# Optimization experiments

Hardware: AMD Instinct MI355X
Metric: run time of the kernel (lower is better)

Reference implementation:

```python
import jax, jax.numpy as jnp
import numpy as np

N_U, N_I, D, L, Q, N_E, B = 100000, 50000, 128, 2, 5, 1000000, 4096
TEMP, LAMBDA1, DROPOUT = 0.2, 0.2, 0.2


def setup_inputs() -> dict:
    key = jax.random.key(0)
    ks = jax.random.split(key, 14)
    s = 1.0 / np.sqrt(D)
    E_u_0 = jax.random.normal(ks[0], (N_U, D), dtype=jnp.float32) * s
    E_i_0 = jax.random.normal(ks[1], (N_I, D), dtype=jnp.float32) * s
    W_s = jax.random.normal(ks[2], (L, D, D), dtype=jnp.float32) * s
    # truncated-SVD factors of adj_norm (rank Q)
    u_mul_s = jax.random.normal(ks[3], (N_U, Q), dtype=jnp.float32) * 0.01
    v_mul_s = jax.random.normal(ks[4], (N_I, Q), dtype=jnp.float32) * 0.01
    ut = jax.random.normal(ks[5], (Q, N_U), dtype=jnp.float32) * 0.01
    vt = jax.random.normal(ks[6], (Q, N_I), dtype=jnp.float32) * 0.01
    # normalized bipartite adjacency in COO form
    adj_rows = jax.random.randint(ks[7], (N_E,), 0, N_U)
    adj_cols = jax.random.randint(ks[8], (N_E,), 0, N_I)
    adj_vals = jax.random.uniform(ks[9], (N_E,), dtype=jnp.float32) * 0.01
    uids = jax.random.randint(ks[10], (B,), 0, N_U)
    iids = jax.random.randint(ks[11], (B,), 0, N_I)
    pos = jax.random.randint(ks[12], (B,), 0, N_I)
    neg = jax.random.randint(ks[13], (B,), 0, N_I)
    return dict(E_u_0=E_u_0, E_i_0=E_i_0, W_s=W_s, u_mul_s=u_mul_s,
                v_mul_s=v_mul_s, ut=ut, vt=vt, adj_vals=adj_vals,
                adj_rows=adj_rows, adj_cols=adj_cols,
                uids=uids, iids=iids, pos=pos, neg=neg)


def _normalize(x):
    n = jnp.linalg.norm(x, axis=1, keepdims=True)
    return x / jnp.maximum(n, 1e-12)


def reference(E_u_0, E_i_0, W_s, u_mul_s, v_mul_s, ut, vt, adj_vals,
              adj_rows, adj_cols, uids, iids, pos, neg):
    act = lambda x: jax.nn.leaky_relu(x, 0.5)
    rkey = jax.random.key(42)
    keep_p = 1.0 - DROPOUT
    E_u, E_i = E_u_0, E_i_0
    E_u_sum, E_i_sum = E_u_0, E_i_0
    Z_u_list, Z_i_list, G_u_list, G_i_list = [], [], [], []
    for layer in range(L):
        k1, k2, rkey = jax.random.split(rkey, 3)
        # two independent sparse dropouts (as in the original, one per spmm)
        v1 = jnp.where(jax.random.bernoulli(k1, keep_p, (N_E,)), adj_vals / keep_p, 0.0)
        v2 = jnp.where(jax.random.bernoulli(k2, keep_p, (N_E,)), adj_vals / keep_p, 0.0)
        # spmm: gather item/user rows, scale by edge val, scatter-add
        Z_u = act(jax.ops.segment_sum(v1[:, None] * E_i[adj_cols], adj_rows, num_segments=N_U))
        Z_i = act(jax.ops.segment_sum(v2[:, None] * E_u[adj_rows], adj_cols, num_segments=N_I))
        # SVD global propagation (low-rank)
        G_u = act(u_mul_s @ (vt @ E_i))
        G_i = act(v_mul_s @ (ut @ E_u))
        E_u = Z_u + E_u
        E_i = Z_i + E_i
        E_u_sum = E_u_sum + E_u
        E_i_sum = E_i_sum + E_i
        Z_u_list.append(Z_u); Z_i_list.append(Z_i)
        G_u_list.append(G_u); G_i_list.append(G_i)

    # InfoNCE contrastive loss per layer
    loss_s = jnp.float32(0.0)
    for l in range(L):
        km1, km2, rkey = jax.random.split(rkey, 3)
        u_mask = (jax.random.uniform(km1, (uids.shape[0],)) > 0.5).astype(jnp.float32)
        gnn_u = _normalize(Z_u_list[l][uids])
        hyper_u = _normalize(G_u_list[l][uids]) @ W_s[l]
        pos_u = jnp.exp(jnp.sum(gnn_u * hyper_u, axis=1) / TEMP)
        neg_u = jnp.sum(jnp.exp(gnn_u @ hyper_u.T / TEMP), axis=1)
        loss_s = loss_s + jnp.sum(-jnp.log(pos_u / (neg_u + 1e-8) + 1e-8) * u_mask)
        i_mask = (jax.random.uniform(km2, (iids.shape[0],)) > 0.5).astype(jnp.float32)
        gnn_i = _normalize(Z_i_list[l][iids])
        hyper_i = _normalize(G_i_list[l][iids]) @ W_s[l]
        pos_i = jnp.exp(jnp.sum(gnn_i * hyper_i, axis=1) / TEMP)
        neg_i = jnp.sum(jnp.exp(gnn_i @ hyper_i.T / TEMP), axis=1)
        loss_s = loss_s + jnp.sum(-jnp.log(pos_i / (neg_i + 1e-8) + 1e-8) * i_mask)

    # BPR loss (vectorized over the per-user loop, one pos/neg per user)
    u_emb = E_u_sum[uids]
    ps = jnp.sum(u_emb * E_i_sum[pos], axis=1)
    ns = jnp.sum(u_emb * E_i_sum[neg], axis=1)
    loss_r = jnp.sum(jax.nn.relu(1.0 - ps + ns)) / B

    loss = loss_r + LAMBDA1 * loss_s
    return loss, loss_r, loss_s
```

## Files before the change

kernel.cpp:

```cpp
#include <hip/hip_runtime.h>
#include <cstdint>
#include <cstddef>

static const int CNU = 100000;
static const int CNI = 50000;
static const int CD  = 128;
static const int CL  = 2;
static const int CQ  = 5;
static const int CNE = 1000000;
static const int CB  = 4096;
#define INV_TEMP 5.0f
#define LAMBDA1 0.2f
#define KEEP_P 0.8f
#define CAP_R 40
#define CAP_C 56
#define NBU 391
#define NBI 196
#define NXCD 8
#define SEGCAP_U 512
#define SEGCAP_I 896
#define QSCALE 655280.0f
#define QSTEP  1.5258902e-6f

typedef unsigned short ushortT;
typedef __attribute__((ext_vector_type(8))) short bf16x8;
typedef __attribute__((ext_vector_type(4))) float f32x4;

__host__ __device__ inline uint32_t rotl32(uint32_t v, int r){ return (v<<r)|(v>>(32-r)); }

__host__ __device__ inline void threefry2x32(uint32_t k0, uint32_t k1, uint32_t x0, uint32_t x1,
                                             uint32_t* o0, uint32_t* o1){
  uint32_t ks0=k0, ks1=k1, ks2=k0^k1^0x1BD11BDAu;
  x0+=ks0; x1+=ks1;
#define TF_R(r) { x0+=x1; x1=rotl32(x1,(r)); x1^=x0; }
  TF_R(13) TF_R(15) TF_R(26) TF_R(6)   x0+=ks1; x1+=ks2+1u;
  TF_R(17) TF_R(29) TF_R(16) TF_R(24)  x0+=ks2; x1+=ks0+2u;
  TF_R(13) TF_R(15) TF_R(26) TF_R(6)   x0+=ks0; x1+=ks1+3u;
  TF_R(17) TF_R(29) TF_R(16) TF_R(24)  x0+=ks1; x1+=ks2+4u;
  TF_R(13) TF_R(15) TF_R(26) TF_R(6)   x0+=ks2; x1+=ks0+5u;
#undef TF_R
  *o0=x0; *o1=x1;
}

static void split3(uint32_t k0, uint32_t k1, uint32_t o[6]){
  uint32_t a,b;
  threefry2x32(k0,k1,0u,3u,&a,&b); o[0]=a; o[3]=b;
  threefry2x32(k0,k1,1u,4u,&a,&b); o[1]=a; o[4]=b;
  threefry2x32(k0,k1,2u,5u,&a,&b); o[2]=a; o[5]=b;
}

__device__ inline float u01(uint32_t b){
  return __uint_as_float((b>>9)|0x3f800000u) - 1.0f;
}
__device__ inline float lrelu(float x){ return x>0.0f ? x : 0.5f*x; }
__device__ inline uint32_t f2bf(float f){
  uint32_t u = __float_as_uint(f);
  u += 0x7fffu + ((u>>16)&1u);
  return u>>16;
}
__device__ inline float bf2f(ushortT s){
  return __uint_as_float(((uint32_t)s)<<16);
}
__device__ inline float bflo(int x){ return __uint_as_float(((uint32_t)x)<<16); }
__device__ inline float bfhi(int x){ return __uint_as_float(((uint32_t)x)&0xffff0000u); }

__device__ inline int keep_draw(uint32_t k0, uint32_t k1, uint32_t e){
  const uint32_t H = CNE/2;
  uint32_t c0 = (e<H)? e : e-H;
  uint32_t r0,r1;
  threefry2x32(k0,k1,c0,c0+H,&r0,&r1);
  uint32_t rw = (e<H)? r0 : r1;
  return (rw < 3435974144u) ? 1 : 0;
}

__device__ inline uint32_t xcc_id(){
  return __builtin_amdgcn_s_getreg((3<<11) | (0<<6) | 20) & (NXCD-1);
}


__global__ void k_cvt(const float* __restrict__ Eu, const float* __restrict__ Ei,
                      ushortT* __restrict__ Eub, ushortT* __restrict__ Eib){
  size_t i = (size_t)blockIdx.x*blockDim.x + threadIdx.x;
  const size_t nu = (size_t)CNU*CD/8;
  const size_t ni = (size_t)CNI*CD/8;
  const float* src; ushortT* dst; size_t j;
  if(i < nu){ src=Eu; dst=Eub; j=i; }
  else if(i < nu+ni){ src=Ei; dst=Eib; j=i-nu; }
  else return;
  const float4* s = (const float4*)(src + j*8);
  float4 a = s[0], b = s[1];
  int4 o;
  o.x = (int)(f2bf(a.x) | (f2bf(a.y)<<16));
  o.y = (int)(f2bf(a.z) | (f2bf(a.w)<<16));
  o.z = (int)(f2bf(b.x) | (f2bf(b.y)<<16));
  o.w = (int)(f2bf(b.z) | (f2bf(b.w)<<16));
  ((int4*)dst)[j] = o;
}

__global__ void k_binfill(const int* __restrict__ rows, const int* __restrict__ cols,
                          const float* __restrict__ vals,
                          int* __restrict__ bcnt_u, int* __restrict__ bcnt_i,
                          int2* __restrict__ bin_u, int2* __restrict__ bin_i,
                          uint32_t ka00, uint32_t ka01, uint32_t ka10, uint32_t ka11,
                          uint32_t kb00, uint32_t kb01, uint32_t kb10, uint32_t kb11){
  int e = blockIdx.x*blockDim.x + threadIdx.x;
  if(e >= CNE) return;
  int xid = (int)xcc_id();
  int r = rows[e], c = cols[e];
  float v = vals[e] * (1.0f/KEEP_P);
  uint32_t q = (uint32_t)(v*QSCALE + 0.5f);
  if(q > 8191u) q = 8191u;
  uint32_t ue = (uint32_t)e;
  uint32_t d0r = keep_draw(ka00, ka01, ue);
  uint32_t d1r = keep_draw(ka10, ka11, ue);
  uint32_t d0c = keep_draw(kb00, kb01, ue);
  uint32_t d1c = keep_draw(kb10, kb11, ue);
  {
    int seg = (r>>8)*NXCD + xid;
    int slot = atomicAdd(&bcnt_u[seg*16], 1);
    if(slot < SEGCAP_U){
      int2 p; p.x = c | ((r&255)<<17); p.y = (int)((d0r<<14)|(d1r<<13)|q);
      bin_u[(size_t)seg*SEGCAP_U + slot] = p;
    }
  }
  {
    int seg = (c>>8)*NXCD + xid;
    int slot = atomicAdd(&bcnt_i[seg*16], 1);
    if(slot < SEGCAP_I){
      int2 p; p.x = r | ((c&255)<<17); p.y = (int)((d0c<<14)|(d1c<<13)|q);
      bin_i[(size_t)seg*SEGCAP_I + slot] = p;
    }
  }
}

__global__ __launch_bounds__(256) void k_build(
    const int* __restrict__ bcnt_u, const int2* __restrict__ bin_u,
    const int* __restrict__ bcnt_i, const int2* __restrict__ bin_i,
    int* __restrict__ cnt_u, uint32_t* __restrict__ pad_u,
    int* __restrict__ cnt_i, uint32_t* __restrict__ pad_i){
  __shared__ int rc[256];
  __shared__ uint32_t lpad[256*CAP_C];
  bool user = blockIdx.x < NBU;
  int bin  = user ? blockIdx.x : blockIdx.x - NBU;
  int N    = user ? CNU : CNI;
  int CAP  = user ? CAP_R : CAP_C;
  int scap = user ? SEGCAP_U : SEGCAP_I;
  const int*  bcnt = user ? bcnt_u : bcnt_i;
  const int2* bino = user ? bin_u : bin_i;
  int* cnto = user ? cnt_u : cnt_i;
  uint32_t* pado = user ? pad_u : pad_i;
  int base = bin<<8;
  int nrows = N - base; if(nrows > 256) nrows = 256;
  int t = threadIdx.x;
  rc[t] = 0;
  __syncthreads();
#pragma unroll
  for(int sgi=0; sgi<NXCD; sgi++){
    int seg = bin*NXCD + sgi;
    int cnt = bcnt[seg*16];
    if(cnt > scap) cnt = scap;
    const int2* bins = bino + (size_t)seg*scap;
    for(int i=t; i<cnt; i+=256){
      int2 p = bins[i];
      int local = ((uint32_t)p.x) >> 17;
      uint32_t gi = (uint32_t)p.x & 0x1FFFFu;
      int slot = atomicAdd(&rc[local], 1);
      if(slot < CAP) lpad[local*CAP + slot] = (gi<<15) | (uint32_t)p.y;
    }
  }
  __syncthreads();
  if(t < nrows){ int n = rc[t]; cnto[base+t] = n>CAP ? CAP : n; }
  int tot4 = (nrows*CAP) >> 2;
  int4* dst = (int4*)(pado + (size_t)base*CAP);
  const int4* src = (const int4*)lpad;
  for(int i4=t; i4<tot4; i4+=256) dst[i4] = src[i4];
}


__global__ __launch_bounds__(256) void k_spmm(
    const int* __restrict__ cnt_u, const uint32_t* __restrict__ pad_u,
    const int* __restrict__ cnt_i, const uint32_t* __restrict__ pad_i,
    const ushortT* __restrict__ Eu_in, const ushortT* __restrict__ Ei_in,
    ushortT* __restrict__ Eu_out, ushortT* __restrict__ Ei_out, int layer){
  __shared__ int2 meta[4][64];
  int wid = threadIdx.x>>6;
  int w = blockIdx.x*4 + wid;
  if(w >= CNU+CNI) return;
  int lane = threadIdx.x & 63;
  bool user = (w < CNU);
  const int*      cnt = user ? cnt_u : cnt_i;
  const uint32_t* pad = user ? pad_u : pad_i;
  int cap             = user ? CAP_R : CAP_C;
  const ushortT* X    = user ? Ei_in : Eu_in;
  const ushortT* Ein  = user ? Eu_in : Ei_in;
  ushortT* Eout       = user ? Eu_out : Ei_out;
  int row = user ? w : (w - CNU);
  int n = cnt[row]; if(n > cap) n = cap;
  const uint32_t* base = pad + (size_t)row*cap;
  int s = lane>>4, l16 = lane&15;

  int2 mm = make_int2(0,0);
  if(lane < n){
    uint32_t mw = base[lane];
    uint32_t keep = (mw >> (14-layer)) & 1u;
    float vv = keep ? (float)(mw & 0x1FFFu) * QSTEP : 0.0f;
    mm.x = (int)(mw >> 15);
    mm.y = __float_as_int(vv);
  }
  meta[wid][lane] = mm;

  float acc[8];
#pragma unroll
  for(int k=0;k<8;k++) acc[k]=0.0f;
  int np = (n+3)>>2;
  for(int i=0;i<np;i++){
    int2 md = meta[wid][i*4+s];
    float vv = __int_as_float(md.y);
    if(vv != 0.0f){
      int4 xv = *(const int4*)(X + (size_t)md.x*CD + l16*8);
      acc[0] += vv*bflo(xv.x); acc[1] += vv*bfhi(xv.x);
      acc[2] += vv*bflo(xv.y); acc[3] += vv*bfhi(xv.y);
      acc[4] += vv*bflo(xv.z); acc[5] += vv*bfhi(xv.z);
      acc[6] += vv*bflo(xv.w); acc[7] += vv*bfhi(xv.w);
    }
  }
#pragma unroll
  for(int k=0;k<8;k++){
    acc[k] += __shfl_xor(acc[k], 16);
    acc[k] += __shfl_xor(acc[k], 32);
  }
  if(s==0){
    int4 ev = *(const int4*)(Ein + (size_t)row*CD + l16*8);
    int4 o;
    o.x = (int)(f2bf(bflo(ev.x)+lrelu(acc[0])) | (f2bf(bfhi(ev.x)+lrelu(acc[1]))<<16));
    o.y = (int)(f2bf(bflo(ev.y)+lrelu(acc[2])) | (f2bf(bfhi(ev.y)+lrelu(acc[3]))<<16));
    o.z = (int)(f2bf(bflo(ev.z)+lrelu(acc[4])) | (f2bf(bfhi(ev.z)+lrelu(acc[5]))<<16));
    o.w = (int)(f2bf(bflo(ev.w)+lrelu(acc[6])) | (f2bf(bfhi(ev.w)+lrelu(acc[7]))<<16));
    *(int4*)(Eout + (size_t)row*CD + l16*8) = o;
  }
}

#define NCH_I 196
#define NCH_U 391
__global__ __launch_bounds__(256) void k_vtE2(const float* __restrict__ vt, const float* __restrict__ ut,
                       const ushortT* __restrict__ Ei, const ushortT* __restrict__ Eu,
                       float* __restrict__ Tu, float* __restrict__ Ti){
  bool sideU = blockIdx.x >= NCH_I;
  int chunk = sideU ? (blockIdx.x - NCH_I) : blockIdx.x;
  const float* M   = sideU ? ut : vt;
  const ushortT* X = sideU ? Eu : Ei;
  float* T         = sideU ? Ti : Tu;
  int N            = sideU ? CNU : CNI;
  int base = chunk*256;
  int t = threadIdx.x;
  int rg = t>>4, dg = t&15;
  float acc[CQ][8];
#pragma unroll
  for(int q=0;q<CQ;q++)
#pragma unroll
    for(int j=0;j<8;j++) acc[q][j]=0.0f;
  for(int rr=rg; rr<256; rr+=16){
    int r = base+rr;
    if(r >= N) break;
    int4 xv = ((const int4*)(X + (size_t)r*CD))[dg];
    float x[8];
    x[0]=bflo(xv.x); x[1]=bfhi(xv.x); x[2]=bflo(xv.y); x[3]=bfhi(xv.y);
    x[4]=bflo(xv.z); x[5]=bfhi(xv.z); x[6]=bflo(xv.w); x[7]=bfhi(xv.w);
#pragma unroll
    for(int q=0;q<CQ;q++){
      float m = M[(size_t)q*N + r];
#pragma unroll
      for(int j=0;j<8;j++) acc[q][j] += m*x[j];
    }
  }
#pragma unroll
  for(int q=0;q<CQ;q++)
#pragma unroll
    for(int j=0;j<8;j++){
      float v = acc[q][j];
      v += __shfl_xor(v, 16);
      v += __shfl_xor(v, 32);
      acc[q][j] = v;
    }
  __shared__ float red[4][656];
  int wv = t>>6;
  int lane = t&63;
  if(lane < 16){
#pragma unroll
    for(int q=0;q<CQ;q++)
#pragma unroll
      for(int j=0;j<8;j++)
        red[wv][dg*41 + q*8 + j] = acc[q][j];
  }
  __syncthreads();
  for(int i=t; i<CQ*128; i+=256){
    int q = i>>7, rem = i&127;
    int dgi = rem>>3, j = rem&7;
    int idx = dgi*41 + q*8 + j;
    float s = red[0][idx] + red[1][idx] + red[2][idx] + red[3][idx];
    atomicAdd(&T[i], s);
  }
}

__global__ void k_hyper2(const int* __restrict__ uids, const int* __restrict__ iids,
                         const float* __restrict__ u_mul_s, const float* __restrict__ v_mul_s,
                         const float* __restrict__ Tu, const float* __restrict__ Ti,
                         const float* __restrict__ W,
                         ushortT* __restrict__ hu, ushortT* __restrict__ hi){
  int side = blockIdx.x >> 12;
  int b    = blockIdx.x & 4095;
  const int* ids = side ? iids : uids;
  const float* ms = side ? v_mul_s : u_mul_s;
  const float* T  = side ? Ti : Tu;
  ushortT* outp = side ? hi : hu;
  int d = threadIdx.x;
  int id = ids[b];
  float g = 0.0f;
#pragma unroll
  for(int q=0;q<CQ;q++) g += ms[(size_t)id*CQ+q]*T[q*128+d];
  g = lrelu(g);
  __shared__ float red[128];
  __shared__ float gn[128];
  red[d]=g*g; __syncthreads();
  for(int s=64;s>0;s>>=1){ if(d<s) red[d]+=red[d+s]; __syncthreads(); }
  float nrm = sqrtf(red[0]);
  gn[d] = g / fmaxf(nrm, 1e-12f);
  __syncthreads();
  float h=0.0f;
  for(int k=0;k<128;k++) h += gn[k]*W[k*128+d];
  outp[(size_t)b*128+d]=(ushortT)f2bf(h);
}

__global__ void k_gnn2(const int* __restrict__ uids, const int* __restrict__ iids,
                       const ushortT* __restrict__ EuN, const ushortT* __restrict__ EuO,
                       const ushortT* __restrict__ EiN, const ushortT* __restrict__ EiO,
                       ushortT* __restrict__ gu, ushortT* __restrict__ gi){
  int side = blockIdx.x >> 12;
  int b    = blockIdx.x & 4095;
  const int* ids = side ? iids : uids;
  const ushortT* En = side ? EiN : EuN;
  const ushortT* Eo = side ? EiO : EuO;
  ushortT* outp = side ? gi : gu;
  int d = threadIdx.x;
  int id = ids[b];
  float z = bf2f(En[(size_t)id*CD+d]) - bf2f(Eo[(size_t)id*CD+d]);
  __shared__ float red[128];
  red[d]=z*z; __syncthreads();
  for(int s=64;s>0;s>>=1){ if(d<s) red[d]+=red[d+s]; __syncthreads(); }
  outp[(size_t)b*CD+d] = (ushortT)f2bf(z / fmaxf(sqrtf(red[0]), 1e-12f));
}

__global__ void k_gacc3(const int* __restrict__ uids, const int* __restrict__ pids,
                        const int* __restrict__ nids,
                        const ushortT* __restrict__ Eu, const ushortT* __restrict__ Ei,
                        float* __restrict__ usum, float* __restrict__ iposb,
                        float* __restrict__ inegb, int init){
  int side = blockIdx.x >> 12;
  int b    = blockIdx.x & 4095;
  const int* ids = (side==0)? uids : (side==1)? pids : nids;
  const ushortT* E = (side==0)? Eu : Ei;
  float* S = (side==0)? usum : (side==1)? iposb : inegb;
  int d = threadIdx.x;
  float v = bf2f(E[(size_t)ids[b]*CD+d]);
  if(init) S[(size_t)b*CD+d]=v;
  else     S[(size_t)b*CD+d]+=v;
}

__global__ __launch_bounds__(256) void k_nce_mfma(const ushortT* __restrict__ gnnb,
                                                  const ushortT* __restrict__ hypb,
                                                  float* __restrict__ neg){
  int c = blockIdx.z;
  const ushortT* G = gnnb + (size_t)c*CB*CD;
  const ushortT* H = hypb + (size_t)c*CB*CD;
  int wid  = threadIdx.x >> 6;
  int lane = threadIdx.x & 63;
  int lr = lane & 15;
  int lk = lane >> 4;
  int rb = blockIdx.x*256 + wid*64;
  int cc = blockIdx.y*512;

  bf16x8 a[4][4];
#pragma unroll
  for(int rt=0;rt<4;rt++)
#pragma unroll
    for(int ks=0;ks<4;ks++)
      a[rt][ks] = *(const bf16x8*)(G + (size_t)(rb+rt*16+lr)*CD + ks*32 + lk*8);

  float rsum[4][4];
#pragma unroll
  for(int rt=0;rt<4;rt++)
#pragma unroll
    for(int r=0;r<4;r++) rsum[rt][r]=0.0f;

  for(int cb=cc; cb<cc+512; cb+=16){
    bf16x8 b[4];
#pragma unroll
    for(int ks=0;ks<4;ks++)
      b[ks] = *(const bf16x8*)(H + (size_t)(cb+lr)*CD + ks*32 + lk*8);
#pragma unroll
    for(int rt=0;rt<4;rt++){
      f32x4 acc = {0.f,0.f,0.f,0.f};
#pragma unroll
      for(int ks=0;ks<4;ks++)
        acc = __builtin_amdgcn_mfma_f32_16x16x32_bf16(a[rt][ks], b[ks], acc, 0,0,0);
#pragma unroll
      for(int r=0;r<4;r++)
        rsum[rt][r] += __expf(acc[r]*INV_TEMP);
    }
  }
#pragma unroll
  for(int rt=0;rt<4;rt++)
#pragma unroll
    for(int r=0;r<4;r++){
      float s = rsum[rt][r];
      s += __shfl_xor(s, 1);
      s += __shfl_xor(s, 2);
      s += __shfl_xor(s, 4);
      s += __shfl_xor(s, 8);
      if(lr==0) atomicAdd(&neg[(size_t)c*CB + rb + rt*16 + lk*4 + r], s);
    }
}

__global__ void k_loss(const ushortT* __restrict__ gnnb, const ushortT* __restrict__ hypb,
                       const float* __restrict__ neg, float* __restrict__ vbuf,
                       uint32_t k0a,uint32_t k0b,uint32_t k1a,uint32_t k1b,
                       uint32_t k2a,uint32_t k2b,uint32_t k3a,uint32_t k3b){
  int idx = blockIdx.x*4 + (threadIdx.x>>6);
  int lane = threadIdx.x & 63;
  const ushortT* g = gnnb + (size_t)idx*CD + lane*2;
  const ushortT* h = hypb + (size_t)idx*CD + lane*2;
  float s = bf2f(g[0])*bf2f(h[0]) + bf2f(g[1])*bf2f(h[1]);
#pragma unroll
  for(int m=32; m; m>>=1) s += __shfl_xor(s, m);
  if(lane==0){
    int c = idx>>12, j = idx&4095;
    uint32_t ka = (c==0)?k0a:(c==1)?k1a:(c==2)?k2a:k3a;
    uint32_t kb = (c==0)?k0b:(c==1)?k1b:(c==2)?k2b:k3b;
    uint32_t jj = (j<2048)? (uint32_t)j : (uint32_t)(j-2048);
    uint32_t r0,r1;
    threefry2x32(ka,kb,jj,jj+2048u,&r0,&r1);
    uint32_t rw = (j<2048)? r0 : r1;
    float mask = (u01(rw) > 0.5f) ? 1.0f : 0.0f;
    float p = __expf(s*INV_TEMP);
    vbuf[idx] = -logf(p/(neg[idx]+1e-8f)+1e-8f) * mask;
  }
}

__global__ void k_bpr(const float* __restrict__ usum, const float* __restrict__ ipos,
                      const float* __restrict__ ineg, float* __restrict__ rbuf){
  int t = threadIdx.x;
  int lane = t & 63, sub = t >> 6;
  int b = blockIdx.x*4 + sub;
  float2 u  = ((const float2*)(usum + (size_t)b*CD))[lane];
  float2 p  = ((const float2*)(ipos + (size_t)b*CD))[lane];
  float2 nn = ((const float2*)(ineg + (size_t)b*CD))[lane];
  float ps = u.x*p.x + u.y*p.y;
  float ns = u.x*nn.x + u.y*nn.y;
  for(int off=32; off; off>>=1){ ps += __shfl_down(ps,off); ns += __shfl_down(ns,off); }
  if(lane==0){
    float v = 1.0f - ps + ns;
    rbuf[b] = v>0.0f ? v : 0.0f;
  }
}

__global__ void k_final(const float* __restrict__ vbuf, const float* __restrict__ rbuf,
                        float* __restrict__ out){
  int t = threadIdx.x;
  float s=0.0f, r=0.0f;
  for(int i=t; i<4*CB; i+=256) s += vbuf[i];
  for(int i=t; i<CB;   i+=256) r += rbuf[i];
  __shared__ float rs[256], rr[256];
  rs[t]=s; rr[t]=r; __syncthreads();
  for(int o=128;o>0;o>>=1){ if(t<o){ rs[t]+=rs[t+o]; rr[t]+=rr[t+o]; } __syncthreads(); }
  if(t==0){
    float loss_s = rs[0];
    float loss_r = rr[0]/(float)CB;
    out[0] = loss_r + LAMBDA1*loss_s;
    out[1] = loss_r;
    out[2] = loss_s;
  }
}

extern "C" void kernel_launch(void* const* d_in, const int* in_sizes, int n_in,
                              void* d_out, int out_size, void* d_ws, size_t ws_size,
                              hipStream_t stream){
  const float* E_u_0   = (const float*)d_in[0];
  const float* E_i_0   = (const float*)d_in[1];
  const float* W_s     = (const float*)d_in[2];
  const float* u_mul_s = (const float*)d_in[3];
  const float* v_mul_s = (const float*)d_in[4];
  const float* ut      = (const float*)d_in[5];
  const float* vt      = (const float*)d_in[6];
  const float* adj_vals= (const float*)d_in[7];
  const int*   adj_rows= (const int*)d_in[8];
  const int*   adj_cols= (const int*)d_in[9];
  const int*   uids    = (const int*)d_in[10];
  const int*   iids    = (const int*)d_in[11];
  const int*   pos_ids = (const int*)d_in[12];
  const int*   neg_ids = (const int*)d_in[13];
  float* out = (float*)d_out;

  float* ws = (float*)d_ws;
  size_t off = 0;
  auto alloc = [&](size_t n){ float* p = ws + off; off += (n+3)&~(size_t)3; return p; };
  ushortT* Eu0b = (ushortT*)alloc((size_t)CNU*CD/2);
  ushortT* Ei0b = (ushortT*)alloc((size_t)CNI*CD/2);
  ushortT* EuA  = (ushortT*)alloc((size_t)CNU*CD/2);
  ushortT* EuB  = (ushortT*)alloc((size_t)CNU*CD/2);
  ushortT* EiA  = (ushortT*)alloc((size_t)CNI*CD/2);
  ushortT* EiB  = (ushortT*)alloc((size_t)CNI*CD/2);
  float* Tu   = alloc(CQ*128);
  float* Ti   = alloc(CQ*128);
  ushortT* gnnb = (ushortT*)alloc(4*(size_t)CB*CD/2);
  ushortT* hypb = (ushortT*)alloc(4*(size_t)CB*CD/2);
  float* usum = alloc((size_t)CB*CD);
  float* iposb= alloc((size_t)CB*CD);
  float* inegb= alloc((size_t)CB*CD);
  float* negb = alloc(4*CB);
  float* vbuf = alloc(4*CB);
  float* rbuf = alloc(CB);
  int* bcnt_u = (int*)alloc((size_t)NBU*NXCD*16);
  int* bcnt_i = (int*)alloc((size_t)NBI*NXCD*16);
  int2* bin_u = (int2*)alloc((size_t)NBU*NXCD*SEGCAP_U*2);
  int2* bin_i = (int2*)alloc((size_t)NBI*NXCD*SEGCAP_I*2);
  int* cnt_u = (int*)alloc(CNU);
  int* cnt_i = (int*)alloc(CNI);
  uint32_t* pad_u = (uint32_t*)alloc((size_t)CNU*CAP_R);
  uint32_t* pad_i = (uint32_t*)alloc((size_t)CNI*CAP_C);

  uint32_t rk0 = 0u, rk1 = 42u;
  uint32_t kd[CL][2][2];
  uint32_t km[4][2];
  for(int l=0;l<CL;l++){
    uint32_t o[6]; split3(rk0,rk1,o);
    kd[l][0][0]=o[0]; kd[l][0][1]=o[1];
    kd[l][1][0]=o[2]; kd[l][1][1]=o[3];
    rk0=o[4]; rk1=o[5];
  }
  for(int l=0;l<CL;l++){
    uint32_t o[6]; split3(rk0,rk1,o);
    km[l*2+0][0]=o[0]; km[l*2+0][1]=o[1];
    km[l*2+1][0]=o[2]; km[l*2+1][1]=o[3];
    rk0=o[4]; rk1=o[5];
  }

  hipMemsetAsync(bcnt_u, 0, (size_t)NBU*NXCD*16*sizeof(int), stream);
  hipMemsetAsync(bcnt_i, 0, (size_t)NBI*NXCD*16*sizeof(int), stream);
  hipMemsetAsync(Tu, 0, CQ*128*sizeof(float), stream);
  hipMemsetAsync(Ti, 0, CQ*128*sizeof(float), stream);
  hipMemsetAsync(negb, 0, 4*CB*sizeof(float), stream);

  {
    size_t tot = ((size_t)CNU+CNI)*CD/8;
    k_cvt<<<(int)((tot+255)/256),256,0,stream>>>(E_u_0, E_i_0, Eu0b, Ei0b);
  }
  k_binfill<<<(CNE+255)/256,256,0,stream>>>(adj_rows, adj_cols, adj_vals,
      bcnt_u, bcnt_i, bin_u, bin_i,
      kd[0][0][0],kd[0][0][1], kd[1][0][0],kd[1][0][1],
      kd[0][1][0],kd[0][1][1], kd[1][1][0],kd[1][1][1]);
  k_build<<<NBU+NBI,256,0,stream>>>(bcnt_u, bin_u, bcnt_i, bin_i,
      cnt_u, pad_u, cnt_i, pad_i);

  k_gacc3<<<3*CB,128,0,stream>>>(uids, pos_ids, neg_ids, Eu0b, Ei0b,
                                 usum, iposb, inegb, 1);

  const ushortT* Eu_cur = Eu0b;
  const ushortT* Ei_cur = Ei0b;
  ushortT* Eu_next_bufs[2] = {EuA, EuB};
  ushortT* Ei_next_bufs[2] = {EiA, EiB};

  for(int l=0;l<CL;l++){
    ushortT* Eu_next = Eu_next_bufs[l];
    ushortT* Ei_next = Ei_next_bufs[l];

    k_spmm<<<(CNU+CNI+3)/4,256,0,stream>>>(
        cnt_u, pad_u, cnt_i, pad_i,
        Eu_cur, Ei_cur, Eu_next, Ei_next, l);

    k_vtE2<<<NCH_I+NCH_U,256,0,stream>>>(vt, ut, Ei_cur, Eu_cur, Tu, Ti);

    const float* Wl = W_s + (size_t)l*CD*CD;
    k_hyper2<<<2*CB,128,0,stream>>>(uids, iids, u_mul_s, v_mul_s, Tu, Ti, Wl,
        hypb + (size_t)(l*2+0)*CB*CD, hypb + (size_t)(l*2+1)*CB*CD);

    k_gnn2<<<2*CB,128,0,stream>>>(uids, iids, Eu_next, Eu_cur, Ei_next, Ei_cur,
        gnnb + (size_t)(l*2+0)*CB*CD, gnnb + (size_t)(l*2+1)*CB*CD);

    Eu_cur = Eu_next; Ei_cur = Ei_next;

    k_gacc3<<<3*CB,128,0,stream>>>(uids, pos_ids, neg_ids, Eu_cur, Ei_cur,
                                   usum, iposb, inegb, 0);

    if(l+1<CL){
      hipMemsetAsync(Tu, 0, CQ*128*sizeof(float), stream);
      hipMemsetAsync(Ti, 0, CQ*128*sizeof(float), stream);
    }
  }

  dim3 gnce(CB/256, CB/512, 4);
  k_nce_mfma<<<gnce,256,0,stream>>>(gnnb, hypb, negb);

  k_loss<<<4*CB/4,256,0,stream>>>(gnnb, hypb, negb, vbuf,
      km[0][0],km[0][1], km[1][0],km[1][1], km[2][0],km[2][1], km[3][0],km[3][1]);
  k_bpr<<<CB/4,256,0,stream>>>(usum, iposb, inegb, rbuf);
  k_final<<<1,256,0,stream>>>(vbuf, rbuf, out);
}
```

Measured before the change: 483.5 us.

## Merge setup, per-layer, and tail stages into fewer heterogeneous-grid kernels

Several small kernels are combined into block-range-dispatched kernels. Bin filling, bf16 conversion and the initial BPR gather become one setup kernel. SpMM and the low-rank vt·E projection share one per-layer kernel, and hyper, gnn-normalisation and the BPR accumulation share another. The loss and BPR kernels are merged, and the separate memsets are folded into two, with the T buffers made per-layer so no re-zeroing is needed between layers. The goal is to cut launch count and inter-kernel idle time and to let independent stages overlap inside one grid. The cost is larger, more divergent kernels and merged memsets that depend on adjacent allocations.

```diff
diff --git a/kernel.cpp b/kernel.cpp
--- a/kernel.cpp
+++ b/kernel.cpp
@@ -21,6 +21,13 @@
 #define SEGCAP_I 896
 #define QSCALE 655280.0f
 #define QSTEP  1.5258902e-6f
+#define NCH_I 196
+#define NCH_U 391
+#define NCH   (NCH_I+NCH_U)
+#define NBF   3907
+#define NCVT  2344
+#define NGA   6144
+#define NSPMM 37500
 
 typedef unsigned short ushortT;
 typedef __attribute__((ext_vector_type(8))) short bf16x8;
@@ -77,59 +84,73 @@
   return __builtin_amdgcn_s_getreg((3<<11) | (0<<6) | 20) & (NXCD-1);
 }
 
-
-__global__ void k_cvt(const float* __restrict__ Eu, const float* __restrict__ Ei,
-                      ushortT* __restrict__ Eub, ushortT* __restrict__ Eib){
-  size_t i = (size_t)blockIdx.x*blockDim.x + threadIdx.x;
-  const size_t nu = (size_t)CNU*CD/8;
-  const size_t ni = (size_t)CNI*CD/8;
-  const float* src; ushortT* dst; size_t j;
-  if(i < nu){ src=Eu; dst=Eub; j=i; }
-  else if(i < nu+ni){ src=Ei; dst=Eib; j=i-nu; }
-  else return;
-  const float4* s = (const float4*)(src + j*8);
-  float4 a = s[0], b = s[1];
-  int4 o;
-  o.x = (int)(f2bf(a.x) | (f2bf(a.y)<<16));
-  o.y = (int)(f2bf(a.z) | (f2bf(a.w)<<16));
-  o.z = (int)(f2bf(b.x) | (f2bf(b.y)<<16));
-  o.w = (int)(f2bf(b.z) | (f2bf(b.w)<<16));
-  ((int4*)dst)[j] = o;
-}
-
-__global__ void k_binfill(const int* __restrict__ rows, const int* __restrict__ cols,
-                          const float* __restrict__ vals,
-                          int* __restrict__ bcnt_u, int* __restrict__ bcnt_i,
-                          int2* __restrict__ bin_u, int2* __restrict__ bin_i,
-                          uint32_t ka00, uint32_t ka01, uint32_t ka10, uint32_t ka11,
-                          uint32_t kb00, uint32_t kb01, uint32_t kb10, uint32_t kb11){
-  int e = blockIdx.x*blockDim.x + threadIdx.x;
-  if(e >= CNE) return;
-  int xid = (int)xcc_id();
-  int r = rows[e], c = cols[e];
-  float v = vals[e] * (1.0f/KEEP_P);
-  uint32_t q = (uint32_t)(v*QSCALE + 0.5f);
-  if(q > 8191u) q = 8191u;
-  uint32_t ue = (uint32_t)e;
-  uint32_t d0r = keep_draw(ka00, ka01, ue);
-  uint32_t d1r = keep_draw(ka10, ka11, ue);
-  uint32_t d0c = keep_draw(kb00, kb01, ue);
-  uint32_t d1c = keep_draw(kb10, kb11, ue);
-  {
-    int seg = (r>>8)*NXCD + xid;
-    int slot = atomicAdd(&bcnt_u[seg*16], 1);
-    if(slot < SEGCAP_U){
-      int2 p; p.x = c | ((r&255)<<17); p.y = (int)((d0r<<14)|(d1r<<13)|q);
-      bin_u[(size_t)seg*SEGCAP_U + slot] = p;
-    }
-  }
-  {
-    int seg = (c>>8)*NXCD + xid;
-    int slot = atomicAdd(&bcnt_i[seg*16], 1);
-    if(slot < SEGCAP_I){
-      int2 p; p.x = r | ((c&255)<<17); p.y = (int)((d0c<<14)|(d1c<<13)|q);
-      bin_i[(size_t)seg*SEGCAP_I + slot] = p;
-    }
+__global__ __launch_bounds__(256) void k_setup(
+    const int* __restrict__ rows, const int* __restrict__ cols,
+    const float* __restrict__ vals,
+    int* __restrict__ bcnt_u, int* __restrict__ bcnt_i,
+    int2* __restrict__ bin_u, int2* __restrict__ bin_i,
+    const float* __restrict__ Euf, const float* __restrict__ Eif,
+    ushortT* __restrict__ Eub, ushortT* __restrict__ Eib,
+    const int* __restrict__ uids, const int* __restrict__ pids, const int* __restrict__ nids,
+    float* __restrict__ usum, float* __restrict__ iposb, float* __restrict__ inegb,
+    uint32_t ka00, uint32_t ka01, uint32_t ka10, uint32_t ka11,
+    uint32_t kb00, uint32_t kb01, uint32_t kb10, uint32_t kb11){
+  int t = threadIdx.x;
+  if(blockIdx.x < NBF){
+    int e = blockIdx.x*256 + t;
+    if(e >= CNE) return;
+    int xid = (int)xcc_id();
+    int r = rows[e], c = cols[e];
+    float v = vals[e] * (1.0f/KEEP_P);
+    uint32_t q = (uint32_t)(v*QSCALE + 0.5f);
+    if(q > 8191u) q = 8191u;
+    uint32_t ue = (uint32_t)e;
+    uint32_t d0r = keep_draw(ka00, ka01, ue);
+    uint32_t d1r = keep_draw(ka10, ka11, ue);
+    uint32_t d0c = keep_draw(kb00, kb01, ue);
+    uint32_t d1c = keep_draw(kb10, kb11, ue);
+    {
+      int seg = (r>>8)*NXCD + xid;
+      int slot = atomicAdd(&bcnt_u[seg*16], 1);
+      if(slot < SEGCAP_U){
+        int2 p; p.x = c | ((r&255)<<17); p.y = (int)((d0r<<14)|(d1r<<13)|q);
+        bin_u[(size_t)seg*SEGCAP_U + slot] = p;
+      }
+    }
+    {
+      int seg = (c>>8)*NXCD + xid;
+      int slot = atomicAdd(&bcnt_i[seg*16], 1);
+      if(slot < SEGCAP_I){
+        int2 p; p.x = r | ((c&255)<<17); p.y = (int)((d0c<<14)|(d1c<<13)|q);
+        bin_i[(size_t)seg*SEGCAP_I + slot] = p;
+      }
+    }
+  } else if(blockIdx.x < NBF+NCVT){
+    const size_t nu = (size_t)CNU*CD/8;
+    const size_t M4 = (size_t)(CNU+CNI)*CD/8;
+    size_t i0 = (size_t)(blockIdx.x - NBF)*256 + t;
+    for(size_t i=i0; i<M4; i += (size_t)NCVT*256){
+      const float* src; ushortT* dst; size_t j;
+      if(i < nu){ src=Euf; dst=Eub; j=i; }
+      else{ src=Eif; dst=Eib; j=i-nu; }
+      const float4* s = (const float4*)(src + j*8);
+      float4 a = s[0], b = s[1];
+      int4 o;
+      o.x = (int)(f2bf(a.x) | (f2bf(a.y)<<16));
+      o.y = (int)(f2bf(a.z) | (f2bf(a.w)<<16));
+      o.z = (int)(f2bf(b.x) | (f2bf(b.y)<<16));
+      o.w = (int)(f2bf(b.z) | (f2bf(b.w)<<16));
+      ((int4*)dst)[j] = o;
+    }
+  } else {
+    int item = (blockIdx.x - NBF - NCVT)*2 + (t>>7);
+    int side = item >> 12;
+    int b    = item & 4095;
+    int d    = t & 127;
+    const int* ids = (side==0)? uids : (side==1)? pids : nids;
+    const float* E = (side==0)? Euf : Eif;
+    float* S = (side==0)? usum : (side==1)? iposb : inegb;
+    S[(size_t)b*CD+d] = E[(size_t)ids[b]*CD+d];
   }
 }
 
@@ -176,194 +197,186 @@
   for(int i4=t; i4<tot4; i4+=256) dst[i4] = src[i4];
 }
 
-
-__global__ __launch_bounds__(256) void k_spmm(
+__global__ __launch_bounds__(256) void k_layer_main(
     const int* __restrict__ cnt_u, const uint32_t* __restrict__ pad_u,
     const int* __restrict__ cnt_i, const uint32_t* __restrict__ pad_i,
     const ushortT* __restrict__ Eu_in, const ushortT* __restrict__ Ei_in,
-    ushortT* __restrict__ Eu_out, ushortT* __restrict__ Ei_out, int layer){
+    ushortT* __restrict__ Eu_out, ushortT* __restrict__ Ei_out,
+    const float* __restrict__ vt, const float* __restrict__ ut,
+    float* __restrict__ Tbuf, int layer){
   __shared__ int2 meta[4][64];
-  int wid = threadIdx.x>>6;
-  int w = blockIdx.x*4 + wid;
-  if(w >= CNU+CNI) return;
-  int lane = threadIdx.x & 63;
-  bool user = (w < CNU);
-  const int*      cnt = user ? cnt_u : cnt_i;
-  const uint32_t* pad = user ? pad_u : pad_i;
-  int cap             = user ? CAP_R : CAP_C;
-  const ushortT* X    = user ? Ei_in : Eu_in;
-  const ushortT* Ein  = user ? Eu_in : Ei_in;
-  ushortT* Eout       = user ? Eu_out : Ei_out;
-  int row = user ? w : (w - CNU);
-  int n = cnt[row]; if(n > cap) n = cap;
-  const uint32_t* base = pad + (size_t)row*cap;
-  int s = lane>>4, l16 = lane&15;
-
-  int2 mm = make_int2(0,0);
-  if(lane < n){
-    uint32_t mw = base[lane];
-    uint32_t keep = (mw >> (14-layer)) & 1u;
-    float vv = keep ? (float)(mw & 0x1FFFu) * QSTEP : 0.0f;
-    mm.x = (int)(mw >> 15);
-    mm.y = __float_as_int(vv);
-  }
-  meta[wid][lane] = mm;
-
-  float acc[8];
-#pragma unroll
-  for(int k=0;k<8;k++) acc[k]=0.0f;
-  int np = (n+3)>>2;
-  for(int i=0;i<np;i++){
-    int2 md = meta[wid][i*4+s];
-    float vv = __int_as_float(md.y);
-    if(vv != 0.0f){
-      int4 xv = *(const int4*)(X + (size_t)md.x*CD + l16*8);
-      acc[0] += vv*bflo(xv.x); acc[1] += vv*bfhi(xv.x);
-      acc[2] += vv*bflo(xv.y); acc[3] += vv*bfhi(xv.y);
-      acc[4] += vv*bflo(xv.z); acc[5] += vv*bfhi(xv.z);
-      acc[6] += vv*bflo(xv.w); acc[7] += vv*bfhi(xv.w);
-    }
-  }
-#pragma unroll
-  for(int k=0;k<8;k++){
-    acc[k] += __shfl_xor(acc[k], 16);
-    acc[k] += __shfl_xor(acc[k], 32);
-  }
-  if(s==0){
-    int4 ev = *(const int4*)(Ein + (size_t)row*CD + l16*8);
-    int4 o;
-    o.x = (int)(f2bf(bflo(ev.x)+lrelu(acc[0])) | (f2bf(bfhi(ev.x)+lrelu(acc[1]))<<16));
-    o.y = (int)(f2bf(bflo(ev.y)+lrelu(acc[2])) | (f2bf(bfhi(ev.y)+lrelu(acc[3]))<<16));
-    o.z = (int)(f2bf(bflo(ev.z)+lrelu(acc[4])) | (f2bf(bfhi(ev.z)+lrelu(acc[5]))<<16));
-    o.w = (int)(f2bf(bflo(ev.w)+lrelu(acc[6])) | (f2bf(bfhi(ev.w)+lrelu(acc[7]))<<16));
-    *(int4*)(Eout + (size_t)row*CD + l16*8) = o;
-  }
-}
-
-#define NCH_I 196
-#define NCH_U 391
-__global__ __launch_bounds__(256) void k_vtE2(const float* __restrict__ vt, const float* __restrict__ ut,
-                       const ushortT* __restrict__ Ei, const ushortT* __restrict__ Eu,
-                       float* __restrict__ Tu, float* __restrict__ Ti){
-  bool sideU = blockIdx.x >= NCH_I;
-  int chunk = sideU ? (blockIdx.x - NCH_I) : blockIdx.x;
-  const float* M   = sideU ? ut : vt;
-  const ushortT* X = sideU ? Eu : Ei;
-  float* T         = sideU ? Ti : Tu;
-  int N            = sideU ? CNU : CNI;
-  int base = chunk*256;
+  __shared__ float red[4][656];
   int t = threadIdx.x;
-  int rg = t>>4, dg = t&15;
-  float acc[CQ][8];
-#pragma unroll
-  for(int q=0;q<CQ;q++)
-#pragma unroll
-    for(int j=0;j<8;j++) acc[q][j]=0.0f;
-  for(int rr=rg; rr<256; rr+=16){
-    int r = base+rr;
-    if(r >= N) break;
-    int4 xv = ((const int4*)(X + (size_t)r*CD))[dg];
-    float x[8];
-    x[0]=bflo(xv.x); x[1]=bfhi(xv.x); x[2]=bflo(xv.y); x[3]=bfhi(xv.y);
-    x[4]=bflo(xv.z); x[5]=bfhi(xv.z); x[6]=bflo(xv.w); x[7]=bfhi(xv.w);
-#pragma unroll
-    for(int q=0;q<CQ;q++){
-      float m = M[(size_t)q*N + r];
-#pragma unroll
-      for(int j=0;j<8;j++) acc[q][j] += m*x[j];
-    }
-  }
-#pragma unroll
-  for(int q=0;q<CQ;q++)
-#pragma unroll
-    for(int j=0;j<8;j++){
-      float v = acc[q][j];
-      v += __shfl_xor(v, 16);
-      v += __shfl_xor(v, 32);
-      acc[q][j] = v;
-    }
-  __shared__ float red[4][656];
-  int wv = t>>6;
-  int lane = t&63;
-  if(lane < 16){
+  if(blockIdx.x < NCH){
+    bool sideU = blockIdx.x >= NCH_I;
+    int chunk = sideU ? (blockIdx.x - NCH_I) : blockIdx.x;
+    const float* M   = sideU ? ut : vt;
+    const ushortT* X = sideU ? Eu_in : Ei_in;
+    float* T         = Tbuf + layer*(2*CQ*128) + (sideU?1:0)*(CQ*128);
+    int N            = sideU ? CNU : CNI;
+    int base = chunk*256;
+    int rg = t>>4, dg = t&15;
+    float acc[CQ][8];
 #pragma unroll
     for(int q=0;q<CQ;q++)
 #pragma unroll
-      for(int j=0;j<8;j++)
-        red[wv][dg*41 + q*8 + j] = acc[q][j];
-  }
-  __syncthreads();
-  for(int i=t; i<CQ*128; i+=256){
-    int q = i>>7, rem = i&127;
-    int dgi = rem>>3, j = rem&7;
-    int idx = dgi*41 + q*8 + j;
-    float s = red[0][idx] + red[1][idx] + red[2][idx] + red[3][idx];
-    atomicAdd(&T[i], s);
-  }
-}
-
-__global__ void k_hyper2(const int* __restrict__ uids, const int* __restrict__ iids,
-                         const float* __restrict__ u_mul_s, const float* __restrict__ v_mul_s,
-                         const float* __restrict__ Tu, const float* __restrict__ Ti,
-                         const float* __restrict__ W,
-                         ushortT* __restrict__ hu, ushortT* __restrict__ hi){
-  int side = blockIdx.x >> 12;
-  int b    = blockIdx.x & 4095;
-  const int* ids = side ? iids : uids;
-  const float* ms = side ? v_mul_s : u_mul_s;
-  const float* T  = side ? Ti : Tu;
-  ushortT* outp = side ? hi : hu;
-  int d = threadIdx.x;
-  int id = ids[b];
-  float g = 0.0f;
-#pragma unroll
-  for(int q=0;q<CQ;q++) g += ms[(size_t)id*CQ+q]*T[q*128+d];
-  g = lrelu(g);
+      for(int j=0;j<8;j++) acc[q][j]=0.0f;
+    for(int rr=rg; rr<256; rr+=16){
+      int r = base+rr;
+      if(r >= N) break;
+      int4 xv = ((const int4*)(X + (size_t)r*CD))[dg];
+      float x[8];
+      x[0]=bflo(xv.x); x[1]=bfhi(xv.x); x[2]=bflo(xv.y); x[3]=bfhi(xv.y);
+      x[4]=bflo(xv.z); x[5]=bfhi(xv.z); x[6]=bflo(xv.w); x[7]=bfhi(xv.w);
+#pragma unroll
+      for(int q=0;q<CQ;q++){
+        float m = M[(size_t)q*N + r];
+#pragma unroll
+        for(int j=0;j<8;j++) acc[q][j] += m*x[j];
+      }
+    }
+#pragma unroll
+    for(int q=0;q<CQ;q++)
+#pragma unroll
+      for(int j=0;j<8;j++){
+        float v = acc[q][j];
+        v += __shfl_xor(v, 16);
+        v += __shfl_xor(v, 32);
+        acc[q][j] = v;
+      }
+    int wv = t>>6;
+    int lane = t&63;
+    if(lane < 16){
+#pragma unroll
+      for(int q=0;q<CQ;q++)
+#pragma unroll
+        for(int j=0;j<8;j++)
+          red[wv][dg*41 + q*8 + j] = acc[q][j];
+    }
+    __syncthreads();
+    for(int i=t; i<CQ*128; i+=256){
+      int q = i>>7, rem = i&127;
+      int dgi = rem>>3, j = rem&7;
+      int idx = dgi*41 + q*8 + j;
+      float s = red[0][idx] + red[1][idx] + red[2][idx] + red[3][idx];
+      atomicAdd(&T[i], s);
+    }
+  } else {
+    int wid = t>>6;
+    int w = (blockIdx.x - NCH)*4 + wid;
+    if(w >= CNU+CNI) return;
+    int lane = t & 63;
+    bool user = (w < CNU);
+    const int*      cnt = user ? cnt_u : cnt_i;
+    const uint32_t* pad = user ? pad_u : pad_i;
+    int cap             = user ? CAP_R : CAP_C;
+    const ushortT* X    = user ? Ei_in : Eu_in;
+    const ushortT* Ein  = user ? Eu_in : Ei_in;
+    ushortT* Eout       = user ? Eu_out : Ei_out;
+    int row = user ? w : (w - CNU);
+    int n = cnt[row]; if(n > cap) n = cap;
+    const uint32_t* base = pad + (size_t)row*cap;
+    int s = lane>>4, l16 = lane&15;
+
+    int2 mm = make_int2(0,0);
+    if(lane < n){
+      uint32_t mw = base[lane];
+      uint32_t keep = (mw >> (14-layer)) & 1u;
+      float vv = keep ? (float)(mw & 0x1FFFu) * QSTEP : 0.0f;
+      mm.x = (int)(mw >> 15);
+      mm.y = __float_as_int(vv);
+    }
+    meta[wid][lane] = mm;
+
+    float acc[8];
+#pragma unroll
+    for(int k=0;k<8;k++) acc[k]=0.0f;
+    int np = (n+3)>>2;
+    for(int i=0;i<np;i++){
+      int2 md = meta[wid][i*4+s];
+      float vv = __int_as_float(md.y);
+      if(vv != 0.0f){
+        int4 xv = *(const int4*)(X + (size_t)md.x*CD + l16*8);
+        acc[0] += vv*bflo(xv.x); acc[1] += vv*bfhi(xv.x);
+        acc[2] += vv*bflo(xv.y); acc[3] += vv*bfhi(xv.y);
+        acc[4] += vv*bflo(xv.z); acc[5] += vv*bfhi(xv.z);
+        acc[6] += vv*bflo(xv.w); acc[7] += vv*bfhi(xv.w);
+      }
+    }
+#pragma unroll
+    for(int k=0;k<8;k++){
+      acc[k] += __shfl_xor(acc[k], 16);
+      acc[k] += __shfl_xor(acc[k], 32);
+    }
+    if(s==0){
+      int4 ev = *(const int4*)(Ein + (size_t)row*CD + l16*8);
+      int4 o;
+      o.x = (int)(f2bf(bflo(ev.x)+lrelu(acc[0])) | (f2bf(bfhi(ev.x)+lrelu(acc[1]))<<16));
+      o.y = (int)(f2bf(bflo(ev.y)+lrelu(acc[2])) | (f2bf(bfhi(ev.y)+lrelu(acc[3]))<<16));
+      o.z = (int)(f2bf(bflo(ev.z)+lrelu(acc[4])) | (f2bf(bfhi(ev.z)+lrelu(acc[5]))<<16));
+      o.w = (int)(f2bf(bflo(ev.w)+lrelu(acc[6])) | (f2bf(bfhi(ev.w)+lrelu(acc[7]))<<16));
+      *(int4*)(Eout + (size_t)row*CD + l16*8) = o;
+    }
+  }
+}
+
+__global__ __launch_bounds__(128) void k_sampled(
+    const int* __restrict__ uids, const int* __restrict__ iids,
+    const int* __restrict__ pids, const int* __restrict__ nids,
+    const float* __restrict__ u_mul_s, const float* __restrict__ v_mul_s,
+    const float* __restrict__ Tbuf, const float* __restrict__ W,
+    const ushortT* __restrict__ EuN, const ushortT* __restrict__ EuO,
+    const ushortT* __restrict__ EiN, const ushortT* __restrict__ EiO,
+    ushortT* __restrict__ hu, ushortT* __restrict__ hi,
+    ushortT* __restrict__ gu, ushortT* __restrict__ gi,
+    float* __restrict__ usum, float* __restrict__ iposb, float* __restrict__ inegb,
+    int layer){
   __shared__ float red[128];
   __shared__ float gn[128];
-  red[d]=g*g; __syncthreads();
-  for(int s=64;s>0;s>>=1){ if(d<s) red[d]+=red[d+s]; __syncthreads(); }
-  float nrm = sqrtf(red[0]);
-  gn[d] = g / fmaxf(nrm, 1e-12f);
-  __syncthreads();
-  float h=0.0f;
-  for(int k=0;k<128;k++) h += gn[k]*W[k*128+d];
-  outp[(size_t)b*128+d]=(ushortT)f2bf(h);
-}
-
-__global__ void k_gnn2(const int* __restrict__ uids, const int* __restrict__ iids,
-                       const ushortT* __restrict__ EuN, const ushortT* __restrict__ EuO,
-                       const ushortT* __restrict__ EiN, const ushortT* __restrict__ EiO,
-                       ushortT* __restrict__ gu, ushortT* __restrict__ gi){
-  int side = blockIdx.x >> 12;
-  int b    = blockIdx.x & 4095;
-  const int* ids = side ? iids : uids;
-  const ushortT* En = side ? EiN : EuN;
-  const ushortT* Eo = side ? EiO : EuO;
-  ushortT* outp = side ? gi : gu;
+  int item = blockIdx.x;
   int d = threadIdx.x;
-  int id = ids[b];
-  float z = bf2f(En[(size_t)id*CD+d]) - bf2f(Eo[(size_t)id*CD+d]);
-  __shared__ float red[128];
-  red[d]=z*z; __syncthreads();
-  for(int s=64;s>0;s>>=1){ if(d<s) red[d]+=red[d+s]; __syncthreads(); }
-  outp[(size_t)b*CD+d] = (ushortT)f2bf(z / fmaxf(sqrtf(red[0]), 1e-12f));
-}
-
-__global__ void k_gacc3(const int* __restrict__ uids, const int* __restrict__ pids,
-                        const int* __restrict__ nids,
-                        const ushortT* __restrict__ Eu, const ushortT* __restrict__ Ei,
-                        float* __restrict__ usum, float* __restrict__ iposb,
-                        float* __restrict__ inegb, int init){
-  int side = blockIdx.x >> 12;
-  int b    = blockIdx.x & 4095;
-  const int* ids = (side==0)? uids : (side==1)? pids : nids;
-  const ushortT* E = (side==0)? Eu : Ei;
-  float* S = (side==0)? usum : (side==1)? iposb : inegb;
-  int d = threadIdx.x;
-  float v = bf2f(E[(size_t)ids[b]*CD+d]);
-  if(init) S[(size_t)b*CD+d]=v;
-  else     S[(size_t)b*CD+d]+=v;
+  if(item < 2*CB){
+    int side = item >> 12;
+    int b    = item & 4095;
+    const int* ids = side ? iids : uids;
+    const float* ms = side ? v_mul_s : u_mul_s;
+    const float* T  = Tbuf + layer*(2*CQ*128) + side*(CQ*128);
+    ushortT* outp = side ? hi : hu;
+    int id = ids[b];
+    float g = 0.0f;
+#pragma unroll
+    for(int q=0;q<CQ;q++) g += ms[(size_t)id*CQ+q]*T[q*128+d];
+    g = lrelu(g);
+    red[d]=g*g; __syncthreads();
+    for(int s=64;s>0;s>>=1){ if(d<s) red[d]+=red[d+s]; __syncthreads(); }
+    float nrm = sqrtf(red[0]);
+    gn[d] = g / fmaxf(nrm, 1e-12f);
+    __syncthreads();
+    float h=0.0f;
+    for(int k=0;k<128;k++) h += gn[k]*W[k*128+d];
+    outp[(size_t)b*128+d]=(ushortT)f2bf(h);
+  } else if(item < 4*CB){
+    int j = item - 2*CB;
+    int side = j >> 12;
+    int b    = j & 4095;
+    const int* ids = side ? iids : uids;
+    const ushortT* En = side ? EiN : EuN;
+    const ushortT* Eo = side ? EiO : EuO;
+    ushortT* outp = side ? gi : gu;
+    int id = ids[b];
+    float z = bf2f(En[(size_t)id*CD+d]) - bf2f(Eo[(size_t)id*CD+d]);
+    red[d]=z*z; __syncthreads();
+    for(int s=64;s>0;s>>=1){ if(d<s) red[d]+=red[d+s]; __syncthreads(); }
+    outp[(size_t)b*CD+d] = (ushortT)f2bf(z / fmaxf(sqrtf(red[0]), 1e-12f));
+  } else {
+    int j = item - 4*CB;
+    int side = j >> 12;
+    int b    = j & 4095;
+    const int* ids = (side==0)? uids : (side==1)? pids : nids;
+    const ushortT* E = (side==0)? EuN : EiN;
+    float* S = (side==0)? usum : (side==1)? iposb : inegb;
+    S[(size_t)b*CD+d] += bf2f(E[(size_t)ids[b]*CD+d]);
+  }
 }
 
 __global__ __launch_bounds__(256) void k_nce_mfma(const ushortT* __restrict__ gnnb,
@@ -421,45 +434,49 @@
     }
 }
 
-__global__ void k_loss(const ushortT* __restrict__ gnnb, const ushortT* __restrict__ hypb,
-                       const float* __restrict__ neg, float* __restrict__ vbuf,
-                       uint32_t k0a,uint32_t k0b,uint32_t k1a,uint32_t k1b,
-                       uint32_t k2a,uint32_t k2b,uint32_t k3a,uint32_t k3b){
-  int idx = blockIdx.x*4 + (threadIdx.x>>6);
-  int lane = threadIdx.x & 63;
-  const ushortT* g = gnnb + (size_t)idx*CD + lane*2;
-  const ushortT* h = hypb + (size_t)idx*CD + lane*2;
-  float s = bf2f(g[0])*bf2f(h[0]) + bf2f(g[1])*bf2f(h[1]);
-#pragma unroll
-  for(int m=32; m; m>>=1) s += __shfl_xor(s, m);
-  if(lane==0){
-    int c = idx>>12, j = idx&4095;
-    uint32_t ka = (c==0)?k0a:(c==1)?k1a:(c==2)?k2a:k3a;
-    uint32_t kb = (c==0)?k0b:(c==1)?k1b:(c==2)?k2b:k3b;
-    uint32_t jj = (j<2048)? (uint32_t)j : (uint32_t)(j-2048);
-    uint32_t r0,r1;
-    threefry2x32(ka,kb,jj,jj+2048u,&r0,&r1);
-    uint32_t rw = (j<2048)? r0 : r1;
-    float mask = (u01(rw) > 0.5f) ? 1.0f : 0.0f;
-    float p = __expf(s*INV_TEMP);
-    vbuf[idx] = -logf(p/(neg[idx]+1e-8f)+1e-8f) * mask;
-  }
-}
-
-__global__ void k_bpr(const float* __restrict__ usum, const float* __restrict__ ipos,
-                      const float* __restrict__ ineg, float* __restrict__ rbuf){
+__global__ __launch_bounds__(256) void k_tail(
+    const ushortT* __restrict__ gnnb, const ushortT* __restrict__ hypb,
+    const float* __restrict__ neg,
+    const float* __restrict__ usum, const float* __restrict__ ipos,
+    const float* __restrict__ ineg,
+    float* __restrict__ vbuf, float* __restrict__ rbuf,
+    uint32_t k0a,uint32_t k0b,uint32_t k1a,uint32_t k1b,
+    uint32_t k2a,uint32_t k2b,uint32_t k3a,uint32_t k3b){
   int t = threadIdx.x;
-  int lane = t & 63, sub = t >> 6;
-  int b = blockIdx.x*4 + sub;
-  float2 u  = ((const float2*)(usum + (size_t)b*CD))[lane];
-  float2 p  = ((const float2*)(ipos + (size_t)b*CD))[lane];
-  float2 nn = ((const float2*)(ineg + (size_t)b*CD))[lane];
-  float ps = u.x*p.x + u.y*p.y;
-  float ns = u.x*nn.x + u.y*nn.y;
-  for(int off=32; off; off>>=1){ ps += __shfl_down(ps,off); ns += __shfl_down(ns,off); }
-  if(lane==0){
-    float v = 1.0f - ps + ns;
-    rbuf[b] = v>0.0f ? v : 0.0f;
+  if(blockIdx.x < 4*CB/4){
+    int idx = blockIdx.x*4 + (t>>6);
+    int lane = t & 63;
+    const ushortT* g = gnnb + (size_t)idx*CD + lane*2;
+    const ushortT* h = hypb + (size_t)idx*CD + lane*2;
+    float s = bf2f(g[0])*bf2f(h[0]) + bf2f(g[1])*bf2f(h[1]);
+#pragma unroll
+    for(int m=32; m; m>>=1) s += __shfl_xor(s, m);
+    if(lane==0){
+      int c = idx>>12, j = idx&4095;
+      uint32_t ka = (c==0)?k0a:(c==1)?k1a:(c==2)?k2a:k3a;
+      uint32_t kb = (c==0)?k0b:(c==1)?k1b:(c==2)?k2b:k3b;
+      uint32_t jj = (j<2048)? (uint32_t)j : (uint32_t)(j-2048);
+      uint32_t r0,r1;
+      threefry2x32(ka,kb,jj,jj+2048u,&r0,&r1);
+      uint32_t rw = (j<2048)? r0 : r1;
+      float mask = (u01(rw) > 0.5f) ? 1.0f : 0.0f;
+      float p = __expf(s*INV_TEMP);
+      vbuf[idx] = -logf(p/(neg[idx]+1e-8f)+1e-8f) * mask;
+    }
+  } else {
+    int bb = blockIdx.x - 4*CB/4;
+    int lane = t & 63, sub = t >> 6;
+    int b = bb*4 + sub;
+    float2 u  = ((const float2*)(usum + (size_t)b*CD))[lane];
+    float2 p  = ((const float2*)(ipos + (size_t)b*CD))[lane];
+    float2 nn = ((const float2*)(ineg + (size_t)b*CD))[lane];
+    float ps = u.x*p.x + u.y*p.y;
+    float ns = u.x*nn.x + u.y*nn.y;
+    for(int off=32; off; off>>=1){ ps += __shfl_down(ps,off); ns += __shfl_down(ns,off); }
+    if(lane==0){
+      float v = 1.0f - ps + ns;
+      rbuf[b] = v>0.0f ? v : 0.0f;
+    }
   }
 }
 
@@ -509,14 +526,13 @@
   ushortT* EuB  = (ushortT*)alloc((size_t)CNU*CD/2);
   ushortT* EiA  = (ushortT*)alloc((size_t)CNI*CD/2);
   ushortT* EiB  = (ushortT*)alloc((size_t)CNI*CD/2);
-  float* Tu   = alloc(CQ*128);
-  float* Ti   = alloc(CQ*128);
+  float* Tbuf = alloc(2*2*CQ*128);
+  float* negb = alloc(4*CB);
   ushortT* gnnb = (ushortT*)alloc(4*(size_t)CB*CD/2);
   ushortT* hypb = (ushortT*)alloc(4*(size_t)CB*CD/2);
   float* usum = alloc((size_t)CB*CD);
   float* iposb= alloc((size_t)CB*CD);
   float* inegb= alloc((size_t)CB*CD);
-  float* negb = alloc(4*CB);
   float* vbuf = alloc(4*CB);
   float* rbuf = alloc(CB);
   int* bcnt_u = (int*)alloc((size_t)NBU*NXCD*16);
@@ -544,25 +560,18 @@
     rk0=o[4]; rk1=o[5];
   }
 
-  hipMemsetAsync(bcnt_u, 0, (size_t)NBU*NXCD*16*sizeof(int), stream);
-  hipMemsetAsync(bcnt_i, 0, (size_t)NBI*NXCD*16*sizeof(int), stream);
-  hipMemsetAsync(Tu, 0, CQ*128*sizeof(float), stream);
-  hipMemsetAsync(Ti, 0, CQ*128*sizeof(float), stream);
-  hipMemsetAsync(negb, 0, 4*CB*sizeof(float), stream);
-
-  {
-    size_t tot = ((size_t)CNU+CNI)*CD/8;
-    k_cvt<<<(int)((tot+255)/256),256,0,stream>>>(E_u_0, E_i_0, Eu0b, Ei0b);
-  }
-  k_binfill<<<(CNE+255)/256,256,0,stream>>>(adj_rows, adj_cols, adj_vals,
+  hipMemsetAsync(bcnt_u, 0, ((size_t)NBU+NBI)*NXCD*16*sizeof(int), stream);
+  hipMemsetAsync(Tbuf, 0, (2*2*CQ*128 + 4*CB)*sizeof(float), stream);
+
+  k_setup<<<NBF+NCVT+NGA,256,0,stream>>>(adj_rows, adj_cols, adj_vals,
       bcnt_u, bcnt_i, bin_u, bin_i,
+      E_u_0, E_i_0, Eu0b, Ei0b,
+      uids, pos_ids, neg_ids, usum, iposb, inegb,
       kd[0][0][0],kd[0][0][1], kd[1][0][0],kd[1][0][1],
       kd[0][1][0],kd[0][1][1], kd[1][1][0],kd[1][1][1]);
+
   k_build<<<NBU+NBI,256,0,stream>>>(bcnt_u, bin_u, bcnt_i, bin_i,
       cnt_u, pad_u, cnt_i, pad_i);
-
-  k_gacc3<<<3*CB,128,0,stream>>>(uids, pos_ids, neg_ids, Eu0b, Ei0b,
-                                 usum, iposb, inegb, 1);
 
   const ushortT* Eu_cur = Eu0b;
   const ushortT* Ei_cur = Ei0b;
@@ -573,35 +582,28 @@
     ushortT* Eu_next = Eu_next_bufs[l];
     ushortT* Ei_next = Ei_next_bufs[l];
 
-    k_spmm<<<(CNU+CNI+3)/4,256,0,stream>>>(
+    k_layer_main<<<NCH+NSPMM,256,0,stream>>>(
         cnt_u, pad_u, cnt_i, pad_i,
-        Eu_cur, Ei_cur, Eu_next, Ei_next, l);
-
-    k_vtE2<<<NCH_I+NCH_U,256,0,stream>>>(vt, ut, Ei_cur, Eu_cur, Tu, Ti);
+        Eu_cur, Ei_cur, Eu_next, Ei_next,
+        vt, ut, Tbuf, l);
 
     const float* Wl = W_s + (size_t)l*CD*CD;
-    k_hyper2<<<2*CB,128,0,stream>>>(uids, iids, u_mul_s, v_mul_s, Tu, Ti, Wl,
-        hypb + (size_t)(l*2+0)*CB*CD, hypb + (size_t)(l*2+1)*CB*CD);
-
-    k_gnn2<<<2*CB,128,0,stream>>>(uids, iids, Eu_next, Eu_cur, Ei_next, Ei_cur,
-        gnnb + (size_t)(l*2+0)*CB*CD, gnnb + (size_t)(l*2+1)*CB*CD);
+    k_sampled<<<7*CB,128,0,stream>>>(
+        uids, iids, pos_ids, neg_ids, u_mul_s, v_mul_s, Tbuf, Wl,
+        Eu_next, Eu_cur, Ei_next, Ei_cur,
+        hypb + (size_t)(l*2+0)*CB*CD, hypb + (size_t)(l*2+1)*CB*CD,
+        gnnb + (size_t)(l*2+0)*CB*CD, gnnb + (size_t)(l*2+1)*CB*CD,
+        usum, iposb, inegb, l);
 
     Eu_cur = Eu_next; Ei_cur = Ei_next;
-
-    k_gacc3<<<3*CB,128,0,stream>>>(uids, pos_ids, neg_ids, Eu_cur, Ei_cur,
-                                   usum, iposb, inegb, 0);
-
-    if(l+1<CL){
-      hipMemsetAsync(Tu, 0, CQ*128*sizeof(float), stream);
-      hipMemsetAsync(Ti, 0, CQ*128*sizeof(float), stream);
-    }
   }
 
   dim3 gnce(CB/256, CB/512, 4);
   k_nce_mfma<<<gnce,256,0,stream>>>(gnnb, hypb, negb);
 
-  k_loss<<<4*CB/4,256,0,stream>>>(gnnb, hypb, negb, vbuf,
+  k_tail<<<4*CB/4 + CB/4,256,0,stream>>>(gnnb, hypb, negb,
+      usum, iposb, inegb, vbuf, rbuf,
       km[0][0],km[0][1], km[1][0],km[1][1], km[2][0],km[2][1], km[3][0],km[3][1]);
-  k_bpr<<<CB/4,256,0,stream>>>(usum, iposb, inegb, rbuf);
+
   k_final<<<1,256,0,stream>>>(vbuf, rbuf, out);
 }
```

Result: slower. 508.9 us (+5.2%).
